# Kernel optimization log

Measured on AMD Instinct MI355X. Metric: run time of the kernel, lower is better.

The kernel has to match this reference:

```python
import jax, jax.numpy as jnp
import numpy as np

B, N, S = 32, 1000, 200
D, H, DK, FF, NL = 128, 8, 16, 512, 3
HK = H * DK


def _mha(x, Wq, Wk, Wv, Wo, bo):
    # x: [B, L, D]; manual multi-head attention matching the torch code
    Bv, L, _ = x.shape
    q = (x @ Wq).reshape(Bv, L, H, DK).transpose(0, 2, 1, 3)  # [B,H,L,dk]
    k = (x @ Wk).reshape(Bv, L, H, DK).transpose(0, 2, 1, 3)
    v = (x @ Wv).reshape(Bv, L, H, DK).transpose(0, 2, 1, 3)
    score = jnp.einsum('bhid,bhjd->bhij', q, k) / jnp.sqrt(jnp.asarray(DK, x.dtype))
    w = jax.nn.softmax(score, axis=-1)
    o = jnp.einsum('bhij,bhjd->bhid', w, v).transpose(0, 2, 1, 3).reshape(Bv, L, HK)
    return o @ Wo + bo


def _decoder_layer(x, Wq, Wk, Wv, Wo, bo, W1, b1, W2, b2):
    out1 = x + _mha(x, Wq, Wk, Wv, Wo, bo)
    ff = jax.nn.relu(out1 @ W1 + b1) @ W2 + b2
    return out1 + ff


def _forward(data, attention_bias, Wfirst, bfirst, Wlast, blast,
             Wq, Wk, Wv, Wo, bo, W1, b1, W2, b2, Wfin, bfin, sel):
    Bv, Np, Dm = data.shape
    Sn = sel.shape[1]
    bidx = jnp.arange(Bv)
    # _get_new_data: ordered list of unselected node indices, shape [B, N-S]
    mask = jnp.zeros((Bv, Np), bool).at[bidx[:, None], sel].set(True)
    vals = jnp.where(mask, Np, jnp.arange(Np)[None, :])
    unselect = jnp.sort(vals, axis=1)[:, : Np - Sn]            # [B, N-S]
    left = jnp.take_along_axis(data, unselect[:, :, None], axis=1)  # [B, N-S, D]
    # _get_encoding for first / last selected node
    first = data[bidx, sel[:, 0]]
    last = data[bidx, sel[:, -1]]
    ef = first @ Wfirst + bfirst
    el = last @ Wlast + blast
    out = jnp.concatenate([ef[:, None], left, el[:, None]], axis=1)  # [B, N-S+2, D]
    for i in range(Wq.shape[0]):
        out = _decoder_layer(out, Wq[i], Wk[i], Wv[i], Wo[i], bo[i],
                             W1[i], b1[i], W2[i], b2[i])
    logits = (out @ Wfin + bfin)[..., 0]                       # [B, N-S+2]
    # attention bias of current (last selected) node, gathered at unselected
    ab_cur = attention_bias[bidx, sel[:, -1]]                  # [B, N]
    ab_uns = jnp.take_along_axis(ab_cur, unselect, axis=1)     # [B, N-S]
    logits = logits.at[:, 1:-1].add(ab_uns)
    L = logits.shape[1]
    pos = jnp.arange(L)
    end_mask = (pos == 0) | (pos == L - 1)
    logits = jnp.where(end_mask[None, :], -jnp.inf, logits)
    props = jax.nn.softmax(logits, axis=-1)[:, 1:-1]           # [B, N-S]
    props = jnp.where(props <= 1e-5, props + 1e-7, props)
    # scatter back: selected positions -> -2, unselected -> props
    new_props = jnp.full((Bv, Np), -2.0, dtype=data.dtype)
    new_props = new_props.at[bidx[:, None], unselect].set(props)
    return new_props


def setup_inputs() -> dict:
    key = jax.random.key(0)
    ks = jax.random.split(key, 24)
    data = jax.random.normal(ks[0], (B, N, D), jnp.float32)
    # selected_node_list must contain unique indices per row (partial tour)
    sel = jax.vmap(lambda k: jax.random.permutation(k, N))(
        jax.random.split(ks[1], B))[:, :S].astype(jnp.int32)
    attention_bias = jax.random.normal(ks[2], (B, N, N), jnp.float32)

    def lin(k, shape, fan_in):
        return jax.random.normal(k, shape, jnp.float32) / np.float32(np.sqrt(fan_in))

    return dict(
        data=data,
        attention_bias=attention_bias,
        Wfirst=lin(ks[3], (D, D), D), bfirst=jnp.zeros((D,), jnp.float32),
        Wlast=lin(ks[4], (D, D), D), blast=jnp.zeros((D,), jnp.float32),
        Wq=lin(ks[5], (NL, D, HK), D),
        Wk=lin(ks[6], (NL, D, HK), D),
        Wv=lin(ks[7], (NL, D, HK), D),
        Wo=lin(ks[8], (NL, HK, D), HK), bo=jnp.zeros((NL, D), jnp.float32),
        W1=lin(ks[9], (NL, D, FF), D), b1=jnp.zeros((NL, FF), jnp.float32),
        W2=lin(ks[10], (NL, FF, D), FF), b2=jnp.zeros((NL, D), jnp.float32),
        Wfin=lin(ks[11], (D, 1), D), bfin=jnp.zeros((1,), jnp.float32),
        selected_node_list=sel,
    )


def reference(data, attention_bias, Wfirst, bfirst, Wlast, blast,
              Wq, Wk, Wv, Wo, bo, W1, b1, W2, b2, Wfin, bfin,
              selected_node_list):
    return _forward(data, attention_bias, Wfirst, bfirst, Wlast, blast,
                    Wq, Wk, Wv, Wo, bo, W1, b1, W2, b2, Wfin, bfin,
                    selected_node_list)
```

## Files before the change

### kernel.cpp

```cpp
#include <hip/hip_runtime.h>
#include <hip/hip_bf16.h>
#include <math.h>

#define NB 32
#define NN 1000
#define SS 200
#define DD 128
#define HH 8
#define DKK 16
#define FFD 512
#define NLAYER 3
#define LQ 802
#define MROWS (NB*LQ)
#define NBLK64 (MROWS/64)
#define NQT 26
#define NQT64 13
#define HSTR 516
#define TSTR 132

typedef __attribute__((ext_vector_type(8))) short short8;
typedef __attribute__((ext_vector_type(4))) short short4v;
typedef __attribute__((ext_vector_type(16))) float f32x16;

static __device__ __forceinline__ unsigned short f2bf(float x) {
  union { float f; unsigned int u; } v; v.f = x;
  unsigned int r = v.u + 0x7fff + ((v.u >> 16) & 1);
  return (unsigned short)(r >> 16);
}

#define WCH 196608
__global__ __launch_bounds__(256) void k_wconv(const float* __restrict__ Wq, const float* __restrict__ Wk,
                       const float* __restrict__ Wv, const float* __restrict__ Wo,
                       const float* __restrict__ W1, const float* __restrict__ W2,
                       unsigned short* __restrict__ WtQKV, unsigned short* __restrict__ Wot,
                       unsigned short* __restrict__ W1t, unsigned short* __restrict__ W2t) {
  int e = blockIdx.x*256 + threadIdx.x;
  if (e >= 3*WCH) return;
  int layer = e / WCH, r = e - layer*WCH;
  if (r < 49152) {
    int n = r >> 7, k = r & 127;
    int sect = n >> 7, nn = n & 127;
    const float* W = (sect == 0) ? Wq : (sect == 1) ? Wk : Wv;
    WtQKV[layer*49152 + r] = f2bf(W[layer*16384 + k*128 + nn]);
  } else if (r < 65536) {
    int r2 = r - 49152;
    int n = r2 >> 7, k = r2 & 127;
    Wot[layer*16384 + r2] = f2bf(Wo[layer*16384 + k*128 + n]);
  } else if (r < 131072) {
    int r2 = r - 65536;
    int n = r2 >> 7, k = r2 & 127;
    W1t[layer*65536 + r2] = f2bf(W1[layer*65536 + k*512 + n]);
  } else {
    int r2 = r - 131072;
    int n = r2 >> 9, k = r2 & 511;
    W2t[layer*65536 + r2] = f2bf(W2[layer*65536 + k*128 + n]);
  }
}

__global__ __launch_bounds__(1024) void k_unselect(const int* __restrict__ sel,
                                                   int* __restrict__ unselect,
                                                   int* __restrict__ pos) {
  int b = blockIdx.x;
  int n = threadIdx.x;
  __shared__ int bufA[1024];
  __shared__ int bufB[1024];
  bufA[n] = (n < NN) ? 1 : 0;
  __syncthreads();
  if (n < SS) bufA[sel[b*SS + n]] = 0;
  __syncthreads();
  int flag = bufA[n];
  int* src = bufA; int* dst = bufB;
  for (int off = 1; off < 1024; off <<= 1) {
    int v = src[n];
    if (n >= off) v += src[n - off];
    __syncthreads();
    dst[n] = v;
    __syncthreads();
    int* tp = src; src = dst; dst = tp;
  }
  if (n < NN) {
    if (flag) {
      int j = src[n] - 1;
      unselect[b*800 + j] = n;
      pos[b*NN + n] = j + 1;
    } else {
      pos[b*NN + n] = -1;
    }
  }
}

__global__ __launch_bounds__(128) void k_embed_ends(const float* __restrict__ data,
                       const int* __restrict__ sel,
                       const float* __restrict__ Wfirst, const float* __restrict__ bfirst,
                       const float* __restrict__ Wlast, const float* __restrict__ blast,
                       float* __restrict__ X, unsigned short* __restrict__ Xbf) {
  int which = blockIdx.x, b = blockIdx.y, d = threadIdx.x;
  int l = (which == 0) ? 0 : LQ-1;
  __shared__ float xr[DD];
  int src = sel[b*SS + (which == 0 ? 0 : SS-1)];
  const float* W    = (which == 0) ? Wfirst : Wlast;
  const float* bias = (which == 0) ? bfirst : blast;
  xr[d] = data[((size_t)b*NN + src)*DD + d];
  __syncthreads();
  float acc = bias[d];
  #pragma unroll 4
  for (int k = 0; k < DD; ++k) acc += xr[k] * W[k*DD + d];
  size_t off = ((size_t)(b*LQ + l))*DD + d;
  X[off] = acc;
  Xbf[off] = f2bf(acc);
}

__global__ __launch_bounds__(256) void k_embed_mid(const float* __restrict__ data,
                       const int* __restrict__ unselect,
                       float* __restrict__ X, unsigned short* __restrict__ Xbf) {
  int e = blockIdx.x*256 + threadIdx.x;
  int r = e >> 5;
  int c4 = (e & 31) * 4;
  int b = r / 800, j = r - b*800;
  int nidx = unselect[r];
  const float4 v = *(const float4*)&data[((size_t)b*NN + nidx)*DD + c4];
  size_t off = ((size_t)(b*LQ + 1 + j))*DD + c4;
  *(float4*)&X[off] = v;
  unsigned short p0 = f2bf(v.x), p1 = f2bf(v.y), p2 = f2bf(v.z), p3 = f2bf(v.w);
  ushort4 pk; pk.x = p0; pk.y = p1; pk.z = p2; pk.w = p3;
  *(ushort4*)&Xbf[off] = pk;
}

__global__ __launch_bounds__(256) void k_qkv_mfma(const unsigned short* __restrict__ Xbf,
                       const unsigned short* __restrict__ Wt,
                       unsigned short* __restrict__ Qb, unsigned short* __restrict__ Kb,
                       unsigned short* __restrict__ Vb) {
  int row0 = blockIdx.x * 64;
  int t = threadIdx.x, wave = t >> 6, lane = t & 63;
  int col = lane & 31, half = lane >> 5;
  short8 a[2][8];
  const unsigned short* xb = Xbf + (size_t)(row0 + col)*DD + half*8;
  #pragma unroll
  for (int mi = 0; mi < 2; ++mi)
    #pragma unroll
    for (int s = 0; s < 8; ++s)
      a[mi][s] = *(const short8*)(xb + (size_t)mi*32*DD + s*16);
  #pragma unroll
  for (int nn = 0; nn < 3; ++nn) {
    int ni = wave*3 + nn;
    short8 bfr[8];
    const unsigned short* wb = Wt + (size_t)(ni*32 + col)*DD + half*8;
    #pragma unroll
    for (int s = 0; s < 8; ++s) bfr[s] = *(const short8*)(wb + s*16);
    f32x16 acc0 = {0.f,0.f,0.f,0.f,0.f,0.f,0.f,0.f,0.f,0.f,0.f,0.f,0.f,0.f,0.f,0.f};
    f32x16 acc1 = {0.f,0.f,0.f,0.f,0.f,0.f,0.f,0.f,0.f,0.f,0.f,0.f,0.f,0.f,0.f,0.f};
    #pragma unroll
    for (int s = 0; s < 8; ++s) {
      acc0 = __builtin_amdgcn_mfma_f32_32x32x16_bf16(a[0][s], bfr[s], acc0, 0, 0, 0);
      acc1 = __builtin_amdgcn_mfma_f32_32x32x16_bf16(a[1][s], bfr[s], acc1, 0, 0, 0);
    }
    int n = ni*32 + col;
    int sect = n >> 7, nc = n & 127;
    int h = nc >> 4, d = nc & 15;
    #pragma unroll
    for (int mi = 0; mi < 2; ++mi) {
      const f32x16& acc = mi ? acc1 : acc0;
      #pragma unroll
      for (int r = 0; r < 16; ++r) {
        int m = row0 + mi*32 + (r&3) + 8*(r>>2) + 4*half;
        int b_ = m / LQ, l = m - b_*LQ;
        size_t bh = (size_t)(b_*HH + h);
        float v = acc[r];
        if (sect == 0)      Qb[(bh*LQ + l)*DKK + d] = f2bf(v * 0.25f);
        else if (sect == 1) Kb[(bh*LQ + l)*DKK + d] = f2bf(v);
        else                Vb[(bh*LQ + l)*DKK + d] = f2bf(v);
      }
    }
  }
}

__global__ __launch_bounds__(256) void k_attn3(const unsigned short* __restrict__ Q,
                       const unsigned short* __restrict__ K,
                       const unsigned short* __restrict__ Vb,
                       unsigned short* __restrict__ Obf) {
  int bid = blockIdx.x;
  int g = bid & 7, i = bid >> 3;
  int bhg = i / NQT64, qt = i - bhg*NQT64;
  int bh = bhg*8 + g;
  int b = bh >> 3, h = bh & 7;
  int q0 = qt*64;
  size_t bhLQ = (size_t)bh * LQ;
  int t = threadIdx.x;
  int wave = t >> 6, lane = t & 63;
  int col = lane & 31;
  int half = lane >> 5;
  bool hb = (half != 0);

  __shared__ float mw[2][4][32];
  __shared__ float sw[2][4][32];
  __shared__ float sfin[2][32];
  __shared__ float ored[2][4][16][32];
  __shared__ float osum[2][32][17];

  int q0c = q0 + col;      if (q0c > LQ-1) q0c = LQ-1;
  int q1c = q0 + 32 + col; if (q1c > LQ-1) q1c = LQ-1;
  short8 bQ0 = *(const short8*)&Q[(bhLQ + q0c)*DKK + half*8];
  short8 bQ1 = *(const short8*)&Q[(bhLQ + q1c)*DKK + half*8];

  f32x16 oacc0 = {0.f,0.f,0.f,0.f,0.f,0.f,0.f,0.f,0.f,0.f,0.f,0.f,0.f,0.f,0.f,0.f};
  f32x16 oacc1 = oacc0;
  float runm0 = -INFINITY, runs0 = 0.f;
  float runm1 = -INFINITY, runs1 = 0.f;

  for (int kt = wave; kt < NQT; kt += 4) {
    int key0 = kt*32;
    int keyA = key0 + col; if (keyA > LQ-1) keyA = LQ-1;
    short8 aK = *(const short8*)&K[(bhLQ + keyA)*DKK + half*8];
    short8 aV0 = {0,0,0,0,0,0,0,0};
    short8 aV1 = {0,0,0,0,0,0,0,0};
    if (col < 16) {
      const unsigned short* vbase = Vb + bhLQ*DKK + col;
      #pragma unroll
      for (int j = 0; j < 8; ++j) {
        int k1 = key0 + half*8 + j;      if (k1 > LQ-1) k1 = LQ-1;
        int k2 = key0 + 16 + half*8 + j; if (k2 > LQ-1) k2 = LQ-1;
        aV0[j] = (short)vbase[(size_t)k1*DKK];
        aV1[j] = (short)vbase[(size_t)k2*DKK];
      }
    }
    bool full = (key0 + 31 < LQ);

    auto process = [&](const short8& bQ, f32x16& oacc, float& runm, float& runs) {
      f32x16 c = {0.f,0.f,0.f,0.f,0.f,0.f,0.f,0.f,0.f,0.f,0.f,0.f,0.f,0.f,0.f,0.f};
      c = __builtin_amdgcn_mfma_f32_32x32x16_bf16(aK, bQ, c, 0, 0, 0);
      float tm;
      if (full) {
        tm = c[0];
        #pragma unroll
        for (int r = 1; r < 16; ++r) tm = fmaxf(tm, c[r]);
      } else {
        tm = -INFINITY;
        #pragma unroll
        for (int r = 0; r < 16; ++r) {
          int key = key0 + (r&3) + 8*(r>>2) + 4*half;
          if (key < LQ) tm = fmaxf(tm, c[r]);
        }
      }
      tm = fmaxf(tm, __shfl_xor(tm, 32, 64));
      float mnew = fmaxf(runm, tm);
      float scale = __expf(runm - mnew);
      runs *= scale;
      #pragma unroll
      for (int r = 0; r < 8; ++r) oacc[r] *= scale;
      runm = mnew;
      float p[16];
      if (full) {
        #pragma unroll
        for (int r = 0; r < 16; ++r) p[r] = __expf(c[r] - mnew);
      } else {
        #pragma unroll
        for (int r = 0; r < 16; ++r) {
          int key = key0 + (r&3) + 8*(r>>2) + 4*half;
          p[r] = (key < LQ) ? __expf(c[r] - mnew) : 0.f;
        }
      }
      float ts = 0.f;
      #pragma unroll
      for (int r = 0; r < 16; ++r) ts += p[r];
      runs += ts;
      unsigned int pk[8];
      #pragma unroll
      for (int j = 0; j < 8; ++j) {
        unsigned int ua = __float_as_uint(p[2*j]);
        unsigned int ub = __float_as_uint(p[2*j+1]);
        pk[j] = (ua >> 16) | (ub & 0xffff0000u);
      }
      int Y0 = __shfl_xor((int)(hb ? pk[0] : pk[2]), 32, 64);
      int Y1 = __shfl_xor((int)(hb ? pk[1] : pk[3]), 32, 64);
      int Y2 = __shfl_xor((int)(hb ? pk[4] : pk[6]), 32, 64);
      int Y3 = __shfl_xor((int)(hb ? pk[5] : pk[7]), 32, 64);
      union { int4 i4; short8 s8; } fA, fB;
      fA.i4.x = hb ? Y0 : (int)pk[0];
      fA.i4.y = hb ? Y1 : (int)pk[1];
      fA.i4.z = hb ? (int)pk[2] : Y0;
      fA.i4.w = hb ? (int)pk[3] : Y1;
      fB.i4.x = hb ? Y2 : (int)pk[4];
      fB.i4.y = hb ? Y3 : (int)pk[5];
      fB.i4.z = hb ? (int)pk[6] : Y2;
      fB.i4.w = hb ? (int)pk[7] : Y3;
      oacc = __builtin_amdgcn_mfma_f32_32x32x16_bf16(aV0, fA.s8, oacc, 0, 0, 0);
      oacc = __builtin_amdgcn_mfma_f32_32x32x16_bf16(aV1, fB.s8, oacc, 0, 0, 0);
    };
    process(bQ0, oacc0, runm0, runs0);
    process(bQ1, oacc1, runm1, runs1);
  }

  float m2v[2], fsv[2];
  #pragma unroll
  for (int u = 0; u < 2; ++u) {
    float runm = u ? runm1 : runm0;
    float runs = u ? runs1 : runs0;
    float pm = __shfl_xor(runm, 32, 64);
    float ps = __shfl_xor(runs, 32, 64);
    float m2 = fmaxf(runm, pm);
    float fself = __expf(runm - m2);
    float s2 = runs*fself + ps*__expf(pm - m2);
    if (half == 0) { mw[u][wave][col] = m2; sw[u][wave][col] = s2; }
    m2v[u] = m2; fsv[u] = fself;
  }
  __syncthreads();
  #pragma unroll
  for (int u = 0; u < 2; ++u) {
    float M = fmaxf(fmaxf(mw[u][0][col], mw[u][1][col]), fmaxf(mw[u][2][col], mw[u][3][col]));
    float S = sw[u][0][col]*__expf(mw[u][0][col]-M) + sw[u][1][col]*__expf(mw[u][1][col]-M)
            + sw[u][2][col]*__expf(mw[u][2][col]-M) + sw[u][3][col]*__expf(mw[u][3][col]-M);
    float fw = __expf(m2v[u] - M) * fsv[u];
    const f32x16& oacc = u ? oacc1 : oacc0;
    #pragma unroll
    for (int r = 0; r < 8; ++r) {
      int dv = (r&3) + 8*(r>>2) + 4*half;
      ored[u][wave][dv][col] = oacc[r] * fw;
    }
    if (wave == 0 && half == 0) sfin[u][col] = S;
  }
  __syncthreads();
  {
    int qq = t & 31, dv0 = t >> 5;
    #pragma unroll
    for (int u = 0; u < 2; ++u)
      #pragma unroll
      for (int k = 0; k < 2; ++k) {
        int dv = dv0 + 8*k;
        osum[u][qq][dv] = ored[u][0][dv][qq] + ored[u][1][dv][qq]
                        + ored[u][2][dv][qq] + ored[u][3][dv][qq];
      }
  }
  __syncthreads();
  {
    int qs = t >> 3, c2 = (t & 7)*2;
    #pragma unroll
    for (int u = 0; u < 2; ++u) {
      int q = q0 + u*32 + qs;
      if (q < LQ) {
        float invS = 1.f / sfin[u][qs];
        unsigned int lo = f2bf(osum[u][qs][c2]   * invS);
        unsigned int hi = f2bf(osum[u][qs][c2+1] * invS);
        *(unsigned int*)&Obf[((size_t)(b*LQ + q))*DD + h*DKK + c2] = lo | (hi << 16);
      }
    }
  }
}

__global__ __launch_bounds__(256) void k_pff(const unsigned short* __restrict__ Obf,
        const unsigned short* __restrict__ Wot, const float* __restrict__ bo,
        const unsigned short* __restrict__ W1t, const float* __restrict__ b1,
        const unsigned short* __restrict__ W2t, const float* __restrict__ b2,
        float* __restrict__ X, unsigned short* __restrict__ Xbf) {
  __shared__ __align__(16) unsigned short LDSU[64 * HSTR];
  unsigned short* T  = LDSU;
  unsigned short* Hs = LDSU;
  int row0 = blockIdx.x * 64;
  int t = threadIdx.x, wave = t >> 6, lane = t & 63;
  int col = lane & 31, half = lane >> 5;
  int n = wave*32 + col;
  float res[2][16];
  {
    short8 a[2][8];
    const unsigned short* ob = Obf + (size_t)(row0 + col)*DD + half*8;
    #pragma unroll
    for (int mi = 0; mi < 2; ++mi)
      #pragma unroll
      for (int s = 0; s < 8; ++s)
        a[mi][s] = *(const short8*)(ob + (size_t)mi*32*DD + s*16);
    short8 bfr[8];
    const unsigned short* wb = Wot + (size_t)n*DD + half*8;
    #pragma unroll
    for (int s = 0; s < 8; ++s) bfr[s] = *(const short8*)(wb + s*16);
    f32x16 acc0 = {0.f,0.f,0.f,0.f,0.f,0.f,0.f,0.f,0.f,0.f,0.f,0.f,0.f,0.f,0.f,0.f};
    f32x16 acc1 = acc0;
    #pragma unroll
    for (int s = 0; s < 8; ++s) {
      acc0 = __builtin_amdgcn_mfma_f32_32x32x16_bf16(a[0][s], bfr[s], acc0, 0, 0, 0);
      acc1 = __builtin_amdgcn_mfma_f32_32x32x16_bf16(a[1][s], bfr[s], acc1, 0, 0, 0);
    }
    float bv = bo[n];
    #pragma unroll
    for (int mi = 0; mi < 2; ++mi) {
      const f32x16& acc = mi ? acc1 : acc0;
      #pragma unroll
      for (int r = 0; r < 16; ++r) {
        int ml = mi*32 + (r&3) + 8*(r>>2) + 4*half;
        size_t off = (size_t)(row0 + ml)*DD + n;
        res[mi][r] = X[off] + acc[r] + bv;
        T[ml*TSTR + n] = f2bf(res[mi][r]);
      }
    }
  }
  __syncthreads();
  short8 aF[2][8];
  #pragma unroll
  for (int mi = 0; mi < 2; ++mi)
    #pragma unroll
    for (int s = 0; s < 8; ++s) {
      const unsigned short* tp = &T[(mi*32 + col)*TSTR + half*8 + s*16];
      union { short4v h[2]; short8 v; } u;
      u.h[0] = *(const short4v*)tp;
      u.h[1] = *(const short4v*)(tp + 4);
      aF[mi][s] = u.v;
    }
  __syncthreads();
  #pragma unroll
  for (int nn = 0; nn < 4; ++nn) {
    int ni = wave*4 + nn;
    short8 bfr[8];
    const unsigned short* wb = W1t + (size_t)(ni*32 + col)*DD + half*8;
    #pragma unroll
    for (int s = 0; s < 8; ++s) bfr[s] = *(const short8*)(wb + s*16);
    f32x16 acc0 = {0.f,0.f,0.f,0.f,0.f,0.f,0.f,0.f,0.f,0.f,0.f,0.f,0.f,0.f,0.f,0.f};
    f32x16 acc1 = acc0;
    #pragma unroll
    for (int s = 0; s < 8; ++s) {
      acc0 = __builtin_amdgcn_mfma_f32_32x32x16_bf16(aF[0][s], bfr[s], acc0, 0, 0, 0);
      acc1 = __builtin_amdgcn_mfma_f32_32x32x16_bf16(aF[1][s], bfr[s], acc1, 0, 0, 0);
    }
    int nf = ni*32 + col;
    float bv = b1[nf];
    #pragma unroll
    for (int mi = 0; mi < 2; ++mi) {
      const f32x16& acc = mi ? acc1 : acc0;
      #pragma unroll
      for (int r = 0; r < 16; ++r) {
        int ml = mi*32 + (r&3) + 8*(r>>2) + 4*half;
        Hs[ml*HSTR + nf] = f2bf(fmaxf(acc[r] + bv, 0.f));
      }
    }
  }
  __syncthreads();
  f32x16 acc0 = {0.f,0.f,0.f,0.f,0.f,0.f,0.f,0.f,0.f,0.f,0.f,0.f,0.f,0.f,0.f,0.f};
  f32x16 acc1 = acc0;
  const unsigned short* w2b = W2t + (size_t)n*FFD + half*8;
  #pragma unroll 4
  for (int s = 0; s < 32; ++s) {
    int ko = s*16 + half*8;
    union { short4v h[2]; short8 v; } h0, h1;
    const unsigned short* hp0 = &Hs[col*HSTR + ko];
    const unsigned short* hp1 = &Hs[(32 + col)*HSTR + ko];
    h0.h[0] = *(const short4v*)hp0;  h0.h[1] = *(const short4v*)(hp0 + 4);
    h1.h[0] = *(const short4v*)hp1;  h1.h[1] = *(const short4v*)(hp1 + 4);
    short8 bfr = *(const short8*)(w2b + s*16);
    acc0 = __builtin_amdgcn_mfma_f32_32x32x16_bf16(h0.v, bfr, acc0, 0, 0, 0);
    acc1 = __builtin_amdgcn_mfma_f32_32x32x16_bf16(h1.v, bfr, acc1, 0, 0, 0);
  }
  float bv = b2[n];
  #pragma unroll
  for (int mi = 0; mi < 2; ++mi) {
    const f32x16& acc = mi ? acc1 : acc0;
    #pragma unroll
    for (int r = 0; r < 16; ++r) {
      int ml = mi*32 + (r&3) + 8*(r>>2) + 4*half;
      size_t off = (size_t)(row0 + ml)*DD + n;
      float v = res[mi][r] + acc[r] + bv;
      X[off] = v;
      Xbf[off] = f2bf(v);
    }
  }
}

__global__ __launch_bounds__(256) void k_logits(const float* __restrict__ X,
                        const float* __restrict__ Wfin, const float* __restrict__ bfin,
                        float* __restrict__ logits) {
  int t = threadIdx.x, wave = t >> 6, lane = t & 63;
  int row = blockIdx.x*4 + wave;
  float2 xv = *(const float2*)&X[(size_t)row*DD + lane*2];
  float2 wv = *(const float2*)&Wfin[lane*2];
  float v = xv.x*wv.x + xv.y*wv.y;
  #pragma unroll
  for (int off = 32; off > 0; off >>= 1) v += __shfl_down(v, off);
  if (lane == 0) logits[row] = v + bfin[0];
}

__global__ __launch_bounds__(256) void k_final(const float* __restrict__ logits,
                       const float* __restrict__ AB, const int* __restrict__ sel,
                       const int* __restrict__ unselect, const int* __restrict__ pos,
                       float* __restrict__ out) {
  int b = blockIdx.x, t = threadIdx.x;
  __shared__ float sl[800];
  __shared__ float red[256];
  int lastsel = sel[b*SS + SS-1];
  const float* abrow = AB + ((size_t)b*NN + lastsel)*NN;
  for (int j = t; j < 800; j += 256)
    sl[j] = logits[b*LQ + j + 1] + abrow[unselect[b*800 + j]];
  __syncthreads();
  float lm = -INFINITY;
  for (int j = t; j < 800; j += 256) lm = fmaxf(lm, sl[j]);
  red[t] = lm;
  __syncthreads();
  for (int s = 128; s > 0; s >>= 1) {
    if (t < s) red[t] = fmaxf(red[t], red[t+s]);
    __syncthreads();
  }
  float m = red[0];
  __syncthreads();
  float ls = 0.f;
  for (int j = t; j < 800; j += 256) ls += __expf(sl[j] - m);
  red[t] = ls;
  __syncthreads();
  for (int s = 128; s > 0; s >>= 1) {
    if (t < s) red[t] += red[t+s];
    __syncthreads();
  }
  float inv = 1.f / red[0];
  for (int n = t; n < NN; n += 256) {
    int p1 = pos[b*NN + n];
    float v = -2.0f;
    if (p1 >= 0) {
      float p = __expf(sl[p1-1] - m) * inv;
      if (p <= 1e-5f) p += 1e-7f;
      v = p;
    }
    out[(size_t)b*NN + n] = v;
  }
}

extern "C" void kernel_launch(void* const* d_in, const int* in_sizes, int n_in,
                              void* d_out, int out_size, void* d_ws, size_t ws_size,
                              hipStream_t stream) {
  const float* data   = (const float*)d_in[0];
  const float* AB     = (const float*)d_in[1];
  const float* Wfirst = (const float*)d_in[2];
  const float* bfirst = (const float*)d_in[3];
  const float* Wlast  = (const float*)d_in[4];
  const float* blast  = (const float*)d_in[5];
  const float* Wq     = (const float*)d_in[6];
  const float* Wk     = (const float*)d_in[7];
  const float* Wv     = (const float*)d_in[8];
  const float* Wo     = (const float*)d_in[9];
  const float* bo     = (const float*)d_in[10];
  const float* W1     = (const float*)d_in[11];
  const float* b1     = (const float*)d_in[12];
  const float* W2     = (const float*)d_in[13];
  const float* b2     = (const float*)d_in[14];
  const float* Wfin   = (const float*)d_in[15];
  const float* bfin   = (const float*)d_in[16];
  const int*   sel    = (const int*)d_in[17];
  float* out = (float*)d_out;
  (void)in_sizes; (void)n_in; (void)out_size; (void)ws_size;

  char* ws = (char*)d_ws;
  const size_t NELT = (size_t)MROWS * DD;
  int*   UNSEL = (int*)ws;
  int*   POS   = (int*)(ws + 102400);
  float* X     = (float*)(ws + 230400);
  unsigned short* Xbf = (unsigned short*)(X + NELT);
  unsigned short* Ob  = Xbf + NELT;
  unsigned short* Qb  = Ob + NELT;
  unsigned short* Kb  = Qb + (size_t)NB*HH*LQ*DKK;
  unsigned short* Vb  = Kb + (size_t)NB*HH*LQ*DKK;
  unsigned short* WtQKV = Vb + (size_t)NB*HH*LQ*DKK;
  unsigned short* Wot = WtQKV + (size_t)NLAYER*384*128;
  unsigned short* W1t = Wot + (size_t)NLAYER*128*128;
  unsigned short* W2t = W1t + (size_t)NLAYER*512*128;
  float* LOG = (float*)(W2t + (size_t)NLAYER*128*512);

  k_wconv<<<(3*WCH + 255)/256, 256, 0, stream>>>(Wq, Wk, Wv, Wo, W1, W2, WtQKV, Wot, W1t, W2t);
  k_unselect<<<NB, 1024, 0, stream>>>(sel, UNSEL, POS);
  k_embed_ends<<<dim3(2, NB), 128, 0, stream>>>(data, sel, Wfirst, bfirst, Wlast, blast, X, Xbf);
  k_embed_mid<<<3200, 256, 0, stream>>>(data, UNSEL, X, Xbf);
  for (int i = 0; i < NLAYER; ++i) {
    k_qkv_mfma<<<NBLK64, 256, 0, stream>>>(Xbf, WtQKV + (size_t)i*384*128, Qb, Kb, Vb);
    k_attn3<<<NQT64*HH*NB, 256, 0, stream>>>(Qb, Kb, Vb, Ob);
    k_pff<<<NBLK64, 256, 0, stream>>>(Ob, Wot + (size_t)i*128*128, bo + (size_t)i*DD,
                                      W1t + (size_t)i*512*128, b1 + (size_t)i*FFD,
                                      W2t + (size_t)i*128*512, b2 + (size_t)i*DD, X, Xbf);
  }
  k_logits<<<MROWS/4, 256, 0, stream>>>(X, Wfin, bfin, LOG);
  k_final<<<NB, 256, 0, stream>>>(LOG, AB, sel, UNSEL, POS, out);
}
```

Measured before the change: 572.7 us.

## Pad K/V to fixed length and pre-transpose V for vectorized attention loads

```diff
diff --git a/kernel.cpp b/kernel.cpp
--- a/kernel.cpp
+++ b/kernel.cpp
@@ -11,6 +11,8 @@
 #define FFD 512
 #define NLAYER 3
 #define LQ 802
+#define LPAD 832
+#define NPADK (LPAD - LQ)
 #define MROWS (NB*LQ)
 #define NBLK64 (MROWS/64)
 #define NQT 26
@@ -166,17 +168,37 @@
         int b_ = m / LQ, l = m - b_*LQ;
         size_t bh = (size_t)(b_*HH + h);
         float v = acc[r];
-        if (sect == 0)      Qb[(bh*LQ + l)*DKK + d] = f2bf(v * 0.25f);
-        else if (sect == 1) Kb[(bh*LQ + l)*DKK + d] = f2bf(v);
-        else                Vb[(bh*LQ + l)*DKK + d] = f2bf(v);
+        if (sect == 0)      Qb[(bh*LPAD + l)*DKK + d] = f2bf(v * 0.25f);
+        else if (sect == 1) Kb[(bh*LPAD + l)*DKK + d] = f2bf(v);
+        else                Vb[(bh*LPAD + l)*DKK + d] = f2bf(v);
       }
     }
   }
+}
+
+__global__ __launch_bounds__(256) void k_vt(const unsigned short* __restrict__ Vb,
+                                            unsigned short* __restrict__ Vt,
+                                            unsigned short* __restrict__ Kb) {
+  __shared__ unsigned short Lt[16][72];
+  int l0 = blockIdx.x * 64;
+  int bh = blockIdx.y;
+  int t = threadIdx.x;
+  int l = t >> 2, d4 = (t & 3) * 4;
+  ushort4 v = {0,0,0,0};
+  if (l0 + l < LQ) v = *(const ushort4*)&Vb[((size_t)bh*LPAD + l0 + l)*DKK + d4];
+  Lt[d4+0][l] = v.x; Lt[d4+1][l] = v.y; Lt[d4+2][l] = v.z; Lt[d4+3][l] = v.w;
+  __syncthreads();
+  int dk = t >> 4, lq = (t & 15)*4;
+  ushort4 o;
+  o.x = Lt[dk][lq]; o.y = Lt[dk][lq+1]; o.z = Lt[dk][lq+2]; o.w = Lt[dk][lq+3];
+  *(ushort4*)&Vt[((size_t)bh*DKK + dk)*LPAD + l0 + lq] = o;
+  if (blockIdx.x == 12 && t < 240)
+    ((unsigned int*)&Kb[((size_t)bh*LPAD + LQ)*DKK])[t] = 0u;
 }
 
 __global__ __launch_bounds__(256) void k_attn3(const unsigned short* __restrict__ Q,
                        const unsigned short* __restrict__ K,
-                       const unsigned short* __restrict__ Vb,
+                       const unsigned short* __restrict__ Vt,
                        unsigned short* __restrict__ Obf) {
   int bid = blockIdx.x;
   int g = bid & 7, i = bid >> 3;
@@ -184,7 +206,7 @@
   int bh = bhg*8 + g;
   int b = bh >> 3, h = bh & 7;
   int q0 = qt*64;
-  size_t bhLQ = (size_t)bh * LQ;
+  size_t bhL = (size_t)bh * LPAD;
   int t = threadIdx.x;
   int wave = t >> 6, lane = t & 63;
   int col = lane & 31;
@@ -199,8 +221,8 @@
 
   int q0c = q0 + col;      if (q0c > LQ-1) q0c = LQ-1;
   int q1c = q0 + 32 + col; if (q1c > LQ-1) q1c = LQ-1;
-  short8 bQ0 = *(const short8*)&Q[(bhLQ + q0c)*DKK + half*8];
-  short8 bQ1 = *(const short8*)&Q[(bhLQ + q1c)*DKK + half*8];
+  short8 bQ0 = *(const short8*)&Q[(bhL + q0c)*DKK + half*8];
+  short8 bQ1 = *(const short8*)&Q[(bhL + q1c)*DKK + half*8];
 
   f32x16 oacc0 = {0.f,0.f,0.f,0.f,0.f,0.f,0.f,0.f,0.f,0.f,0.f,0.f,0.f,0.f,0.f,0.f};
   f32x16 oacc1 = oacc0;
@@ -209,38 +231,21 @@
 
   for (int kt = wave; kt < NQT; kt += 4) {
     int key0 = kt*32;
-    int keyA = key0 + col; if (keyA > LQ-1) keyA = LQ-1;
-    short8 aK = *(const short8*)&K[(bhLQ + keyA)*DKK + half*8];
+    short8 aK = *(const short8*)&K[(bhL + key0 + col)*DKK + half*8];
     short8 aV0 = {0,0,0,0,0,0,0,0};
     short8 aV1 = {0,0,0,0,0,0,0,0};
     if (col < 16) {
-      const unsigned short* vbase = Vb + bhLQ*DKK + col;
-      #pragma unroll
-      for (int j = 0; j < 8; ++j) {
-        int k1 = key0 + half*8 + j;      if (k1 > LQ-1) k1 = LQ-1;
-        int k2 = key0 + 16 + half*8 + j; if (k2 > LQ-1) k2 = LQ-1;
-        aV0[j] = (short)vbase[(size_t)k1*DKK];
-        aV1[j] = (short)vbase[(size_t)k2*DKK];
-      }
-    }
-    bool full = (key0 + 31 < LQ);
+      const unsigned short* vp = &Vt[((size_t)bh*DKK + col)*LPAD + key0 + half*8];
+      aV0 = *(const short8*)vp;
+      aV1 = *(const short8*)(vp + 16);
+    }
 
     auto process = [&](const short8& bQ, f32x16& oacc, float& runm, float& runs) {
       f32x16 c = {0.f,0.f,0.f,0.f,0.f,0.f,0.f,0.f,0.f,0.f,0.f,0.f,0.f,0.f,0.f,0.f};
       c = __builtin_amdgcn_mfma_f32_32x32x16_bf16(aK, bQ, c, 0, 0, 0);
-      float tm;
-      if (full) {
-        tm = c[0];
-        #pragma unroll
-        for (int r = 1; r < 16; ++r) tm = fmaxf(tm, c[r]);
-      } else {
-        tm = -INFINITY;
-        #pragma unroll
-        for (int r = 0; r < 16; ++r) {
-          int key = key0 + (r&3) + 8*(r>>2) + 4*half;
-          if (key < LQ) tm = fmaxf(tm, c[r]);
-        }
-      }
+      float tm = c[0];
+      #pragma unroll
+      for (int r = 1; r < 16; ++r) tm = fmaxf(tm, c[r]);
       tm = fmaxf(tm, __shfl_xor(tm, 32, 64));
       float mnew = fmaxf(runm, tm);
       float scale = __expf(runm - mnew);
@@ -249,16 +254,8 @@
       for (int r = 0; r < 8; ++r) oacc[r] *= scale;
       runm = mnew;
       float p[16];
-      if (full) {
-        #pragma unroll
-        for (int r = 0; r < 16; ++r) p[r] = __expf(c[r] - mnew);
-      } else {
-        #pragma unroll
-        for (int r = 0; r < 16; ++r) {
-          int key = key0 + (r&3) + 8*(r>>2) + 4*half;
-          p[r] = (key < LQ) ? __expf(c[r] - mnew) : 0.f;
-        }
-      }
+      #pragma unroll
+      for (int r = 0; r < 16; ++r) p[r] = __expf(c[r] - mnew);
       float ts = 0.f;
       #pragma unroll
       for (int r = 0; r < 16; ++r) ts += p[r];
@@ -316,7 +313,8 @@
       int dv = (r&3) + 8*(r>>2) + 4*half;
       ored[u][wave][dv][col] = oacc[r] * fw;
     }
-    if (wave == 0 && half == 0) sfin[u][col] = S;
+    if (wave == 0 && half == 0)
+      sfin[u][col] = S - (float)NPADK * __expf(-M);
   }
   __syncthreads();
   {
@@ -543,15 +541,17 @@
 
   char* ws = (char*)d_ws;
   const size_t NELT = (size_t)MROWS * DD;
+  const size_t KVELT = (size_t)NB*HH*LPAD*DKK;
   int*   UNSEL = (int*)ws;
   int*   POS   = (int*)(ws + 102400);
   float* X     = (float*)(ws + 230400);
   unsigned short* Xbf = (unsigned short*)(X + NELT);
   unsigned short* Ob  = Xbf + NELT;
   unsigned short* Qb  = Ob + NELT;
-  unsigned short* Kb  = Qb + (size_t)NB*HH*LQ*DKK;
-  unsigned short* Vb  = Kb + (size_t)NB*HH*LQ*DKK;
-  unsigned short* WtQKV = Vb + (size_t)NB*HH*LQ*DKK;
+  unsigned short* Kb  = Qb + KVELT;
+  unsigned short* Vb  = Kb + KVELT;
+  unsigned short* Vt  = Vb + KVELT;
+  unsigned short* WtQKV = Vt + KVELT;
   unsigned short* Wot = WtQKV + (size_t)NLAYER*384*128;
   unsigned short* W1t = Wot + (size_t)NLAYER*128*128;
   unsigned short* W2t = W1t + (size_t)NLAYER*512*128;
@@ -563,7 +563,8 @@
   k_embed_mid<<<3200, 256, 0, stream>>>(data, UNSEL, X, Xbf);
   for (int i = 0; i < NLAYER; ++i) {
     k_qkv_mfma<<<NBLK64, 256, 0, stream>>>(Xbf, WtQKV + (size_t)i*384*128, Qb, Kb, Vb);
-    k_attn3<<<NQT64*HH*NB, 256, 0, stream>>>(Qb, Kb, Vb, Ob);
+    k_vt<<<dim3(13, NB*HH), 256, 0, stream>>>(Vb, Vt, Kb);
+    k_attn3<<<NQT64*HH*NB, 256, 0, stream>>>(Qb, Kb, Vt, Ob);
     k_pff<<<NBLK64, 256, 0, stream>>>(Ob, Wot + (size_t)i*128*128, bo + (size_t)i*DD,
                                       W1t + (size_t)i*512*128, b1 + (size_t)i*FFD,
                                       W2t + (size_t)i*128*512, b2 + (size_t)i*DD, X, Xbf);
```

New measurement: 560.8 us. 1.02x faster.
